# Performance work log

Hardware: AMD Instinct MI355X
Metric: run time of the kernel (lower is better)

Reference implementation:

```python
import jax, jax.numpy as jnp
import numpy as np

WL_W = 8  # weight bit-width (wl_weight)
WL_A = 8  # activation bit-width (wl_activate)


def _wage_q(x, bits):
    """WAGE quantizer with straight-through estimator.

    Rounds to a grid of step 1/2^(bits-1) and clips to (-1+delta, 1-delta),
    matching NeuroSim's wage_quantizer Q/C composition and the detach-based
    STE used in QConv2d/QLinear's training (inference=0) path.
    """
    s = 2.0 ** (bits - 1)
    delta = 1.0 / s
    q = jnp.clip(jnp.round(x * s) / s, -1.0 + delta, 1.0 - delta)
    return x + jax.lax.stop_gradient(q - x)


def _qconv(x, w):
    # quantize weights -> 3x3 conv (stride 1, pad 1) -> quantize activations
    wq = _wage_q(w, WL_W)
    y = jax.lax.conv_general_dilated(
        x, wq, window_strides=(1, 1), padding=((1, 1), (1, 1)),
        dimension_numbers=('NCHW', 'OIHW', 'NCHW'))
    return _wage_q(y, WL_A)


def setup_inputs() -> dict:
    key = jax.random.key(0)
    ks = jax.random.split(key, 9)
    x = jax.random.normal(ks[0], (16, 4, 256, 256), dtype=jnp.float32)
    w1 = jax.random.normal(ks[1], (32, 4, 3, 3), dtype=jnp.float32) * 0.2
    ws = {f"w{i}": jax.random.normal(ks[i], (32, 32, 3, 3), dtype=jnp.float32) * 0.1
          for i in range(2, 8)}
    wfc = jax.random.normal(ks[8], (1, 32), dtype=jnp.float32) * 0.2
    return {"x": x, "w1": w1, **ws, "wfc": wfc}


def reference(x, w1, w2, w3, w4, w5, w6, w7, wfc):
    # 7 stacked quantized 3x3 convs, channels 4->32->...->32
    for w in (w1, w2, w3, w4, w5, w6, w7):
        x = _qconv(x, w)                    # [B,32,256,256]
    x = jnp.max(x, axis=(2, 3))             # MaxPool2d(256,256) == global max -> [B,32]
    wq = _wage_q(wfc, WL_W)
    y = x @ wq.T                             # QLinear 32 -> 1, [B,1]
    return _wage_q(y, WL_A)
```

## Files before the change

kernel.cpp:

```cpp
#include <hip/hip_runtime.h>

#define BB 16
#define HH 256
#define WW 256

typedef int i32x4 __attribute__((ext_vector_type(4)));
typedef int i32x16 __attribute__((ext_vector_type(16)));
typedef float f32x16 __attribute__((ext_vector_type(16)));
typedef _Float16 f16x8 __attribute__((ext_vector_type(8)));

__global__ __launch_bounds__(256) void prep_kernel(
    const float* __restrict__ x, const float* __restrict__ w1,
    const float* __restrict__ w2, const float* __restrict__ w3,
    const float* __restrict__ w4, const float* __restrict__ w5,
    const float* __restrict__ w6, const float* __restrict__ w7,
    const float* __restrict__ wfc,
    _Float16* __restrict__ pre, _Float16* __restrict__ frag1,
    signed char* __restrict__ wfr, int* __restrict__ wfcq,
    int* __restrict__ gmax) {
  int bid = blockIdx.x, tid = threadIdx.x;
  if (bid < 4096) {
    int px = bid * 256 + tid;
    int b = px >> 16, rem = px & 65535;
    const float* xp = x + (size_t)b * 4 * 65536 + rem;
    f16x8 o;
#pragma unroll
    for (int ic = 0; ic < 4; ++ic) {
      float v = xp[ic * 65536];
      _Float16 hf = (_Float16)v;
      float r = v - (float)hf;
      o[ic * 2] = hf;
      o[ic * 2 + 1] = (_Float16)r;
    }
    *(f16x8*)(pre + (size_t)px * 8) = o;
  } else if (bid < 4312) {
    int i = (bid - 4096) * 256 + tid;
    int layer = i / 9216, within = i - layer * 9216;
    const float* w = layer == 0 ? w2 : layer == 1 ? w3 : layer == 2 ? w4
                   : layer == 3 ? w5 : layer == 4 ? w6 : w7;
    int t = within >> 10;
    int l = (within >> 4) & 63;
    int j = within & 15;
    int ic = (l >> 5) * 16 + j;
    int oc = l & 31;
    int q = (int)rintf(w[oc * 288 + ic * 9 + t] * 128.0f);
    q = min(127, max(-127, q));
    wfr[(size_t)layer * 9216 + within] = (signed char)q;
  } else {
    for (int p = tid; p < 384; p += 256) {
      int s = p >> 6, l = p & 63;
      int dr = s >> 1, pp = s & 1;
      int oc = l & 31, half = l >> 5;
      int dx = pp * 2 + half;
#pragma unroll
      for (int j = 0; j < 8; ++j) {
        int ic = j >> 1;
        _Float16 v = (_Float16)0.f;
        if (!(pp == 1 && half == 1)) {
          int q = (int)rintf(w1[oc * 36 + ic * 9 + dr * 3 + dx] * 128.0f);
          q = min(127, max(-127, q));
          v = (_Float16)((float)q * 0.0078125f);
        }
        frag1[s * 512 + l * 8 + j] = v;
      }
    }
    if (tid < 32) {
      int q = (int)rintf(wfc[tid] * 128.0f);
      q = min(127, max(-127, q));
      wfcq[tid] = q;
    }
    for (int i2 = tid; i2 < 512; i2 += 256) gmax[i2] = -128;
  }
}

__device__ __forceinline__ int pack4(int q0, int q1, int q2, int q3) {
  return (q0 & 255) | ((q1 & 255) << 8) | ((q2 & 255) << 16) | ((q3 & 255) << 24);
}

__device__ __forceinline__ int quant1(int a) {
  int q = (a + 63 + ((a >> 7) & 1)) >> 7;
  return min(127, max(-127, q));
}

__device__ __forceinline__ int quant_max(const i32x16& acc, int mymax) {
#pragma unroll
  for (int r = 0; r < 16; ++r) mymax = max(mymax, quant1(acc[r]));
  return mymax;
}

__device__ __forceinline__ i32x4 half_swap(int v0, int v1, int v2, int v3, int hi) {
  int s0 = hi ? v0 : v2;
  int s1 = hi ? v1 : v3;
  int r0 = __shfl_xor(s0, 32);
  int r1 = __shfl_xor(s1, 32);
  i32x4 ch;
  ch.x = hi ? r0 : v0;
  ch.y = hi ? v2 : r0;
  ch.z = hi ? r1 : v1;
  ch.w = hi ? v3 : r1;
  return ch;
}

__global__ __launch_bounds__(256) void conv1_mfma_kernel(
    const _Float16* __restrict__ pre, const _Float16* __restrict__ frag1,
    signed char* __restrict__ out) {
  int tid = threadIdx.x;
  int wi = tid >> 6;
  int l = tid & 63;
  int lo = l & 31;
  int hi = l >> 5;
  int b = blockIdx.z;
  int h0 = blockIdx.y * 2;
  int wbase = blockIdx.x * 128 + wi * 32;
  int w = wbase + lo;

  const f16x8* fp = (const f16x8*)frag1;
  f16x8 bf[6];
#pragma unroll
  for (int s = 0; s < 6; ++s) bf[s] = fp[s * 64 + l];

  f32x16 acc0 = {}, acc1 = {};
  const size_t img = (size_t)b * (HH * WW);

#pragma unroll
  for (int r = 0; r < 4; ++r) {
    int yy = h0 - 1 + r;
    bool okr = (unsigned)yy < 256u;
#pragma unroll
    for (int p = 0; p < 2; ++p) {
      int xx = w + p * 2 + hi - 1;
      f16x8 av = {};
      if (okr && !(p == 1 && hi == 1) && ((unsigned)xx < 256u))
        av = *(const f16x8*)(pre + ((img + (size_t)yy * WW + xx) << 3));
      if (r < 3) acc0 = __builtin_amdgcn_mfma_f32_32x32x16_f16(bf[r * 2 + p], av, acc0, 0, 0, 0);
      if (r > 0) acc1 = __builtin_amdgcn_mfma_f32_32x32x16_f16(bf[(r - 1) * 2 + p], av, acc1, 0, 0, 0);
    }
  }

#pragma unroll
  for (int rr = 0; rr < 2; ++rr) {
    const f32x16& acc = rr ? acc1 : acc0;
    int q[16];
#pragma unroll
    for (int r = 0; r < 16; ++r) {
      int t = (int)rintf(acc[r] * 128.0f);
      q[r] = min(127, max(-127, t));
    }
    int v0 = pack4(q[0], q[1], q[2], q[3]);
    int v1 = pack4(q[4], q[5], q[6], q[7]);
    int v2 = pack4(q[8], q[9], q[10], q[11]);
    int v3 = pack4(q[12], q[13], q[14], q[15]);
    i32x4 ch = half_swap(v0, v1, v2, v3, hi);
    *(i32x4*)(out + ((img + (size_t)(h0 + rr) * WW + w) << 5) + hi * 16) = ch;
  }
}

template <int MODE>
__global__ __launch_bounds__(512, 4) void conv_fused_kernel(
    const signed char* __restrict__ in, const signed char* __restrict__ fragA,
    const signed char* __restrict__ fragB, signed char* __restrict__ out,
    int* __restrict__ gmax) {
  __shared__ int Lint[6 * 2 * 256 * 4];
  __shared__ int red[8][32];

  int tid = threadIdx.x;
  int wi = tid >> 6;
  int l = tid & 63;
  int lo = l & 31;
  int hi = l >> 5;
  int b = blockIdx.y;
  int hs = blockIdx.x * 4;
  int w = wi * 32 + lo;
  const size_t img = (size_t)b * (HH * WW);

  const i32x4* fpA = (const i32x4*)fragA;
  i32x4 bw[9];
#pragma unroll
  for (int t = 0; t < 9; ++t) bw[t] = fpA[t * 64 + l];

  auto ldrow = [&](int yy, int dx) -> i32x4 {
    i32x4 r = {};
    int xx = w + dx - 1;
    if (((unsigned)yy < 256u) && ((unsigned)xx < 256u))
      r = *(const i32x4*)(in + ((img + (size_t)yy * WW + xx) << 5) + hi * 16);
    return r;
  };

  auto lds_store_row = [&](const i32x16& acc, int rrel) {
    int v0 = pack4(quant1(acc[0]), quant1(acc[1]), quant1(acc[2]), quant1(acc[3]));
    int v1 = pack4(quant1(acc[4]), quant1(acc[5]), quant1(acc[6]), quant1(acc[7]));
    int v2 = pack4(quant1(acc[8]), quant1(acc[9]), quant1(acc[10]), quant1(acc[11]));
    int v3 = pack4(quant1(acc[12]), quant1(acc[13]), quant1(acc[14]), quant1(acc[15]));
    i32x4 ch = half_swap(v0, v1, v2, v3, hi);
    *(i32x4*)&Lint[((rrel * 2 + hi) * 256 + w) * 4] = ch;
  };

#pragma unroll 1
  for (int p = 0; p < 3; ++p) {
    int ar0 = hs - 1 + 2 * p;
    i32x4 rin[4][3];
#pragma unroll
    for (int rr = 0; rr < 4; ++rr)
#pragma unroll
      for (int dx = 0; dx < 3; ++dx)
        rin[rr][dx] = ldrow(ar0 - 1 + rr, dx);

    i32x16 acc0 = {}, acc1 = {};
#pragma unroll
    for (int t = 0; t < 9; ++t) {
      int dy = t / 3, dx = t % 3;
      acc0 = __builtin_amdgcn_mfma_i32_32x32x32_i8(bw[t], rin[dy][dx], acc0, 0, 0, 0);
      acc1 = __builtin_amdgcn_mfma_i32_32x32x32_i8(bw[t], rin[dy + 1][dx], acc1, 0, 0, 0);
    }
    lds_store_row(acc0, 2 * p);
    lds_store_row(acc1, 2 * p + 1);
  }

  const i32x4* fpB = (const i32x4*)fragB;
#pragma unroll
  for (int t = 0; t < 9; ++t) bw[t] = fpB[t * 64 + l];
  __syncthreads();

  int mymax = -128;
#pragma unroll 1
  for (int p = 0; p < 2; ++p) {
    i32x4 tp[4][3];
#pragma unroll
    for (int rr = 0; rr < 4; ++rr) {
      int rrel = 2 * p + rr;
      int aro = hs - 1 + rrel;
#pragma unroll
      for (int dx = 0; dx < 3; ++dx) {
        int px = w + dx - 1;
        i32x4 v = {};
        if (((unsigned)aro < 256u) && ((unsigned)px < 256u))
          v = *(const i32x4*)&Lint[((rrel * 2 + hi) * 256 + px) * 4];
        tp[rr][dx] = v;
      }
    }
    i32x16 acc0 = {}, acc1 = {};
#pragma unroll
    for (int t = 0; t < 9; ++t) {
      int dy = t / 3, dx = t % 3;
      if (MODE == 1) {
        acc0 = __builtin_amdgcn_mfma_i32_32x32x32_i8(tp[dy][dx], bw[t], acc0, 0, 0, 0);
        acc1 = __builtin_amdgcn_mfma_i32_32x32x32_i8(tp[dy + 1][dx], bw[t], acc1, 0, 0, 0);
      } else {
        acc0 = __builtin_amdgcn_mfma_i32_32x32x32_i8(bw[t], tp[dy][dx], acc0, 0, 0, 0);
        acc1 = __builtin_amdgcn_mfma_i32_32x32x32_i8(bw[t], tp[dy + 1][dx], acc1, 0, 0, 0);
      }
    }
    if (MODE == 0) {
#pragma unroll
      for (int rr = 0; rr < 2; ++rr) {
        const i32x16& acc = rr ? acc1 : acc0;
        int v0 = pack4(quant1(acc[0]), quant1(acc[1]), quant1(acc[2]), quant1(acc[3]));
        int v1 = pack4(quant1(acc[4]), quant1(acc[5]), quant1(acc[6]), quant1(acc[7]));
        int v2 = pack4(quant1(acc[8]), quant1(acc[9]), quant1(acc[10]), quant1(acc[11]));
        int v3 = pack4(quant1(acc[12]), quant1(acc[13]), quant1(acc[14]), quant1(acc[15]));
        i32x4 ch = half_swap(v0, v1, v2, v3, hi);
        *(i32x4*)(out + ((img + (size_t)(hs + 2 * p + rr) * WW + w) << 5) + hi * 16) = ch;
      }
    } else {
      mymax = quant_max(acc1, quant_max(acc0, mymax));
    }
  }

  if (MODE == 1) {
    mymax = max(mymax, __shfl_xor(mymax, 32));
    if (hi == 0) red[wi][lo] = mymax;
    __syncthreads();
    if (tid < 32) {
      int m = -128;
#pragma unroll
      for (int r = 0; r < 8; ++r) m = max(m, red[r][tid]);
      atomicMax(&gmax[b * 32 + tid], m);
    }
  }
}

__global__ void fc_kernel(const int* __restrict__ gmax, const int* __restrict__ wfcq,
                          float* __restrict__ out) {
  int b = threadIdx.x;
  if (b < BB) {
    int acc = 0;
#pragma unroll
    for (int c = 0; c < 32; ++c) acc += gmax[b * 32 + c] * wfcq[c];
    int q = (acc + 63 + ((acc >> 7) & 1)) >> 7;
    q = min(127, max(-127, q));
    out[b] = (float)q * 0.0078125f;
  }
}

extern "C" void kernel_launch(void* const* d_in, const int* in_sizes, int n_in,
                              void* d_out, int out_size, void* d_ws, size_t ws_size,
                              hipStream_t stream) {
  const float* x   = (const float*)d_in[0];
  const float* w1  = (const float*)d_in[1];
  const float* wfc = (const float*)d_in[8];

  char* ws = (char*)d_ws;
  const size_t ACTB = (size_t)BB * HH * WW * 32;
  signed char* A0    = (signed char*)ws;
  signed char* A1    = (signed char*)(ws + ACTB);
  _Float16*    pre   = (_Float16*)A1;
  _Float16*    frag1 = (_Float16*)(ws + 2 * ACTB);
  signed char* wfr   = (signed char*)(ws + 2 * ACTB + 6144);
  int*         wfcq  = (int*)(ws + 2 * ACTB + 6144 + 6 * 9216);
  int*         gmax  = (int*)(ws + 2 * ACTB + 6144 + 6 * 9216 + 128);

  prep_kernel<<<4313, 256, 0, stream>>>(
      x, w1, (const float*)d_in[2], (const float*)d_in[3], (const float*)d_in[4],
      (const float*)d_in[5], (const float*)d_in[6], (const float*)d_in[7],
      wfc, pre, frag1, wfr, wfcq, gmax);

  dim3 gridc1(2, 128, 16);
  conv1_mfma_kernel<<<gridc1, 256, 0, stream>>>(pre, frag1, A0);

  dim3 gf(64, 16);
  conv_fused_kernel<0><<<gf, 512, 0, stream>>>(A0, wfr + 0 * 9216, wfr + 1 * 9216, A1, nullptr);
  conv_fused_kernel<0><<<gf, 512, 0, stream>>>(A1, wfr + 2 * 9216, wfr + 3 * 9216, A0, nullptr);
  conv_fused_kernel<1><<<gf, 512, 0, stream>>>(A0, wfr + 4 * 9216, wfr + 5 * 9216, nullptr, gmax);
  fc_kernel<<<1, 64, 0, stream>>>(gmax, wfcq, (float*)d_out);
}
```

Measured before the change: 138.5 us.

## Store activations in zero-padded 258x258 layout to drop boundary checks

Activations and the fp16 input are stored with a one-pixel zero halo (258x258 per image). Border rows and columns are zeroed once in prep and in an extra pad kernel, so the conv loads run without per-element bounds predicates. The LDS tile gets padded columns too, with invalid rows written as zeros. This costs an extra small kernel launch, slightly more memory, and clamped row pointers that read the padding.

```diff
diff --git a/kernel.cpp b/kernel.cpp
--- a/kernel.cpp
+++ b/kernel.cpp
@@ -3,6 +3,8 @@
 #define BB 16
 #define HH 256
 #define WW 256
+#define PC 258
+#define PP ((size_t)(PC * PC))
 
 typedef int i32x4 __attribute__((ext_vector_type(4)));
 typedef int i32x16 __attribute__((ext_vector_type(16)));
@@ -17,11 +19,12 @@
     const float* __restrict__ wfc,
     _Float16* __restrict__ pre, _Float16* __restrict__ frag1,
     signed char* __restrict__ wfr, int* __restrict__ wfcq,
-    int* __restrict__ gmax) {
+    int* __restrict__ gmax, signed char* __restrict__ A0) {
   int bid = blockIdx.x, tid = threadIdx.x;
   if (bid < 4096) {
     int px = bid * 256 + tid;
     int b = px >> 16, rem = px & 65535;
+    int y = rem >> 8, xc = rem & 255;
     const float* xp = x + (size_t)b * 4 * 65536 + rem;
     f16x8 o;
 #pragma unroll
@@ -32,7 +35,7 @@
       o[ic * 2] = hf;
       o[ic * 2 + 1] = (_Float16)r;
     }
-    *(f16x8*)(pre + (size_t)px * 8) = o;
+    *(f16x8*)(pre + ((size_t)b * PP + (size_t)(y + 1) * PC + (xc + 1)) * 8) = o;
   } else if (bid < 4312) {
     int i = (bid - 4096) * 256 + tid;
     int layer = i / 9216, within = i - layer * 9216;
@@ -46,7 +49,7 @@
     int q = (int)rintf(w[oc * 288 + ic * 9 + t] * 128.0f);
     q = min(127, max(-127, q));
     wfr[(size_t)layer * 9216 + within] = (signed char)q;
-  } else {
+  } else if (bid == 4312) {
     for (int p = tid; p < 384; p += 256) {
       int s = p >> 6, l = p & 63;
       int dr = s >> 1, pp = s & 1;
@@ -70,6 +73,36 @@
       wfcq[tid] = q;
     }
     for (int i2 = tid; i2 < 512; i2 += 256) gmax[i2] = -128;
+  } else {
+    int idx = (bid - 4313) * 256 + tid;
+    if (idx < 16448) {
+      int img = idx / 1028, p = idx - img * 1028;
+      int row, col;
+      if (p < 258) { row = 0; col = p; }
+      else if (p < 516) { row = 257; col = p - 258; }
+      else { int q2 = p - 516; row = 1 + (q2 & 255); col = (q2 >> 8) ? 257 : 0; }
+      size_t off = (size_t)img * PP + (size_t)row * PC + col;
+      f16x8 z16 = {};
+      *(f16x8*)(pre + off * 8) = z16;
+      i32x4 z = {};
+      ((i32x4*)(A0 + off * 32))[0] = z;
+      ((i32x4*)(A0 + off * 32 + 16))[0] = z;
+    }
+  }
+}
+
+__global__ __launch_bounds__(256) void pad_kernel(signed char* __restrict__ A1) {
+  int idx = blockIdx.x * 256 + threadIdx.x;
+  if (idx < 16448) {
+    int img = idx / 1028, p = idx - img * 1028;
+    int row, col;
+    if (p < 258) { row = 0; col = p; }
+    else if (p < 516) { row = 257; col = p - 258; }
+    else { int q2 = p - 516; row = 1 + (q2 & 255); col = (q2 >> 8) ? 257 : 0; }
+    size_t off = (size_t)img * PP + (size_t)row * PC + col;
+    i32x4 z = {};
+    ((i32x4*)(A1 + off * 32))[0] = z;
+    ((i32x4*)(A1 + off * 32 + 16))[0] = z;
   }
 }
 
@@ -120,18 +153,16 @@
   for (int s = 0; s < 6; ++s) bf[s] = fp[s * 64 + l];
 
   f32x16 acc0 = {}, acc1 = {};
-  const size_t img = (size_t)b * (HH * WW);
 
 #pragma unroll
   for (int r = 0; r < 4; ++r) {
-    int yy = h0 - 1 + r;
-    bool okr = (unsigned)yy < 256u;
+    const _Float16* rp = pre + ((size_t)b * PP + (size_t)(h0 + r) * PC) * 8;
 #pragma unroll
     for (int p = 0; p < 2; ++p) {
-      int xx = w + p * 2 + hi - 1;
+      int col = w + p * 2 + hi;
       f16x8 av = {};
-      if (okr && !(p == 1 && hi == 1) && ((unsigned)xx < 256u))
-        av = *(const f16x8*)(pre + ((img + (size_t)yy * WW + xx) << 3));
+      if (!(p == 1 && hi == 1))
+        av = *(const f16x8*)(rp + (size_t)col * 8);
       if (r < 3) acc0 = __builtin_amdgcn_mfma_f32_32x32x16_f16(bf[r * 2 + p], av, acc0, 0, 0, 0);
       if (r > 0) acc1 = __builtin_amdgcn_mfma_f32_32x32x16_f16(bf[(r - 1) * 2 + p], av, acc1, 0, 0, 0);
     }
@@ -151,7 +182,7 @@
     int v2 = pack4(q[8], q[9], q[10], q[11]);
     int v3 = pack4(q[12], q[13], q[14], q[15]);
     i32x4 ch = half_swap(v0, v1, v2, v3, hi);
-    *(i32x4*)(out + ((img + (size_t)(h0 + rr) * WW + w) << 5) + hi * 16) = ch;
+    *(i32x4*)(out + ((size_t)b * PP + (size_t)(h0 + rr + 1) * PC + (w + 1)) * 32 + hi * 16) = ch;
   }
 }
 
@@ -160,7 +191,7 @@
     const signed char* __restrict__ in, const signed char* __restrict__ fragA,
     const signed char* __restrict__ fragB, signed char* __restrict__ out,
     int* __restrict__ gmax) {
-  __shared__ int Lint[6 * 2 * 256 * 4];
+  __shared__ int Lint[6 * 2 * PC * 4];
   __shared__ int red[8][32];
 
   int tid = threadIdx.x;
@@ -171,39 +202,47 @@
   int b = blockIdx.y;
   int hs = blockIdx.x * 4;
   int w = wi * 32 + lo;
-  const size_t img = (size_t)b * (HH * WW);
+
+  if (tid < 24) {
+    int rr = tid >> 2, half = (tid >> 1) & 1, cs = tid & 1;
+    i32x4 z = {};
+    *(i32x4*)&Lint[((rr * 2 + half) * PC + (cs ? 257 : 0)) * 4] = z;
+  }
 
   const i32x4* fpA = (const i32x4*)fragA;
   i32x4 bw[9];
 #pragma unroll
   for (int t = 0; t < 9; ++t) bw[t] = fpA[t * 64 + l];
 
-  auto ldrow = [&](int yy, int dx) -> i32x4 {
-    i32x4 r = {};
-    int xx = w + dx - 1;
-    if (((unsigned)yy < 256u) && ((unsigned)xx < 256u))
-      r = *(const i32x4*)(in + ((img + (size_t)yy * WW + xx) << 5) + hi * 16);
-    return r;
+  int lanep = (w << 5) + (hi << 4);
+
+  auto rowptr = [&](int yy) -> const signed char* {
+    int prow = min(max(yy + 1, 0), 257);
+    return in + ((size_t)b * PP + (size_t)prow * PC) * 32 + lanep;
   };
 
-  auto lds_store_row = [&](const i32x16& acc, int rrel) {
+  auto lds_store_row = [&](const i32x16& acc, int rrel, bool valid) {
     int v0 = pack4(quant1(acc[0]), quant1(acc[1]), quant1(acc[2]), quant1(acc[3]));
     int v1 = pack4(quant1(acc[4]), quant1(acc[5]), quant1(acc[6]), quant1(acc[7]));
     int v2 = pack4(quant1(acc[8]), quant1(acc[9]), quant1(acc[10]), quant1(acc[11]));
     int v3 = pack4(quant1(acc[12]), quant1(acc[13]), quant1(acc[14]), quant1(acc[15]));
     i32x4 ch = half_swap(v0, v1, v2, v3, hi);
-    *(i32x4*)&Lint[((rrel * 2 + hi) * 256 + w) * 4] = ch;
+    if (!valid) ch = i32x4{};
+    *(i32x4*)&Lint[((rrel * 2 + hi) * PC + (w + 1)) * 4] = ch;
   };
 
 #pragma unroll 1
   for (int p = 0; p < 3; ++p) {
     int ar0 = hs - 1 + 2 * p;
+    const signed char* rp[4];
+#pragma unroll
+    for (int rr = 0; rr < 4; ++rr) rp[rr] = rowptr(ar0 - 1 + rr);
     i32x4 rin[4][3];
 #pragma unroll
     for (int rr = 0; rr < 4; ++rr)
 #pragma unroll
       for (int dx = 0; dx < 3; ++dx)
-        rin[rr][dx] = ldrow(ar0 - 1 + rr, dx);
+        rin[rr][dx] = *(const i32x4*)(rp[rr] + dx * 32);
 
     i32x16 acc0 = {}, acc1 = {};
 #pragma unroll
@@ -212,8 +251,8 @@
       acc0 = __builtin_amdgcn_mfma_i32_32x32x32_i8(bw[t], rin[dy][dx], acc0, 0, 0, 0);
       acc1 = __builtin_amdgcn_mfma_i32_32x32x32_i8(bw[t], rin[dy + 1][dx], acc1, 0, 0, 0);
     }
-    lds_store_row(acc0, 2 * p);
-    lds_store_row(acc1, 2 * p + 1);
+    lds_store_row(acc0, 2 * p, (unsigned)ar0 < 256u);
+    lds_store_row(acc1, 2 * p + 1, (unsigned)(ar0 + 1) < 256u);
   }
 
   const i32x4* fpB = (const i32x4*)fragB;
@@ -228,15 +267,9 @@
 #pragma unroll
     for (int rr = 0; rr < 4; ++rr) {
       int rrel = 2 * p + rr;
-      int aro = hs - 1 + rrel;
-#pragma unroll
-      for (int dx = 0; dx < 3; ++dx) {
-        int px = w + dx - 1;
-        i32x4 v = {};
-        if (((unsigned)aro < 256u) && ((unsigned)px < 256u))
-          v = *(const i32x4*)&Lint[((rrel * 2 + hi) * 256 + px) * 4];
-        tp[rr][dx] = v;
-      }
+#pragma unroll
+      for (int dx = 0; dx < 3; ++dx)
+        tp[rr][dx] = *(const i32x4*)&Lint[((rrel * 2 + hi) * PC + (w + dx)) * 4];
     }
     i32x16 acc0 = {}, acc1 = {};
 #pragma unroll
@@ -259,7 +292,7 @@
         int v2 = pack4(quant1(acc[8]), quant1(acc[9]), quant1(acc[10]), quant1(acc[11]));
         int v3 = pack4(quant1(acc[12]), quant1(acc[13]), quant1(acc[14]), quant1(acc[15]));
         i32x4 ch = half_swap(v0, v1, v2, v3, hi);
-        *(i32x4*)(out + ((img + (size_t)(hs + 2 * p + rr) * WW + w) << 5) + hi * 16) = ch;
+        *(i32x4*)(out + ((size_t)b * PP + (size_t)(hs + 2 * p + rr + 1) * PC + (w + 1)) * 32 + hi * 16) = ch;
       }
     } else {
       mymax = quant_max(acc1, quant_max(acc0, mymax));
@@ -300,22 +333,23 @@
   const float* wfc = (const float*)d_in[8];
 
   char* ws = (char*)d_ws;
-  const size_t ACTB = (size_t)BB * HH * WW * 32;
+  const size_t ACTP = (size_t)BB * PP * 32;
   signed char* A0    = (signed char*)ws;
-  signed char* A1    = (signed char*)(ws + ACTB);
+  signed char* A1    = (signed char*)(ws + ACTP);
   _Float16*    pre   = (_Float16*)A1;
-  _Float16*    frag1 = (_Float16*)(ws + 2 * ACTB);
-  signed char* wfr   = (signed char*)(ws + 2 * ACTB + 6144);
-  int*         wfcq  = (int*)(ws + 2 * ACTB + 6144 + 6 * 9216);
-  int*         gmax  = (int*)(ws + 2 * ACTB + 6144 + 6 * 9216 + 128);
-
-  prep_kernel<<<4313, 256, 0, stream>>>(
+  _Float16*    frag1 = (_Float16*)(ws + 2 * ACTP);
+  signed char* wfr   = (signed char*)(ws + 2 * ACTP + 6144);
+  int*         wfcq  = (int*)(ws + 2 * ACTP + 6144 + 6 * 9216);
+  int*         gmax  = (int*)(ws + 2 * ACTP + 6144 + 6 * 9216 + 128);
+
+  prep_kernel<<<4378, 256, 0, stream>>>(
       x, w1, (const float*)d_in[2], (const float*)d_in[3], (const float*)d_in[4],
       (const float*)d_in[5], (const float*)d_in[6], (const float*)d_in[7],
-      wfc, pre, frag1, wfr, wfcq, gmax);
+      wfc, pre, frag1, wfr, wfcq, gmax, A0);
 
   dim3 gridc1(2, 128, 16);
   conv1_mfma_kernel<<<gridc1, 256, 0, stream>>>(pre, frag1, A0);
+  pad_kernel<<<65, 256, 0, stream>>>(A1);
 
   dim3 gf(64, 16);
   conv_fused_kernel<0><<<gf, 512, 0, stream>>>(A0, wfr + 0 * 9216, wfr + 1 * 9216, A1, nullptr);
```

After: 136.2 us. No clear change (-1.7%).
